# Performance work log

Measured on AMD Instinct MI355X. Metric: run time of the kernel, lower is better.

Reference implementation:

```python
import jax, jax.numpy as jnp
import numpy as np

D_MODEL = 4096
N_EXPERTS = 64
LN_EPS = 1e-5


def setup_inputs() -> dict:
    key = jax.random.key(0)
    k_x, k_w, k_b = jax.random.split(key, 3)
    x = jax.random.normal(k_x, (4, 4096, D_MODEL), dtype=jnp.float32)
    # LayerNorm affine params (torch defaults: ones / zeros)
    gamma = jnp.ones((D_MODEL,), dtype=jnp.float32)
    beta = jnp.zeros((D_MODEL,), dtype=jnp.float32)
    # Linear(d_model, n): weight (n, d), bias (n) — kaiming-uniform-ish init
    bound = 1.0 / np.sqrt(D_MODEL)
    W = jax.random.uniform(k_w, (N_EXPERTS, D_MODEL), dtype=jnp.float32, minval=-bound, maxval=bound)
    b = jax.random.uniform(k_b, (N_EXPERTS,), dtype=jnp.float32, minval=-bound, maxval=bound)
    return {"x": x, "gamma": gamma, "beta": beta, "W": W, "b": b, "top_k": 2}


def reference(x, gamma, beta, W, b, top_k):
    # LayerNorm over last dim
    mu = jnp.mean(x, axis=-1, keepdims=True)
    var = jnp.mean(jnp.square(x - mu), axis=-1, keepdims=True)
    xn = (x - mu) * jax.lax.rsqrt(var + LN_EPS) * gamma + beta
    # Gate projection: (B,T,d) @ (d,n) -> (B,T,n)
    logits = jnp.einsum('btd,nd->btn', xn, W) + b
    weights = jax.nn.softmax(logits, axis=-1)  # (B,T,n)
    k = min(int(top_k), weights.shape[-1])
    topk_vals, indices = jax.lax.top_k(weights, k)  # (B,T,k)
    # scatter top-k values back to dense (B,T,n), then renormalize
    onehot = jax.nn.one_hot(indices, weights.shape[-1], dtype=weights.dtype)  # (B,T,k,n)
    sparse_w = jnp.einsum('btkn,btk->btn', onehot, topk_vals)
    sparse_w = sparse_w / (jnp.sum(sparse_w, axis=-1, keepdims=True) + 1e-8)
    # load-balance (entropy) loss on dense weights
    mean_w = jnp.mean(weights, axis=(0, 1))  # (n,)
    lb_loss = -jnp.sum(mean_w * jnp.log(mean_w + 1e-8))
    return sparse_w, indices, lb_loss
```

## Files before the change

kernel.cpp:

```cpp
#include <hip/hip_runtime.h>
#include <math.h>

#define D_MODEL 4096
#define N_EXP   64
#define N_ROWS  16384
#define LN_EPS  1e-5f
#define TMB     64
#define NBLK    (N_ROWS / TMB)

typedef __attribute__((ext_vector_type(4))) float f32x4;
typedef __attribute__((ext_vector_type(8))) short s16x8;

struct U4 { unsigned v[4]; };

__device__ __forceinline__ unsigned pkt(float a, float b) {
  unsigned ua = __builtin_bit_cast(unsigned, a);
  unsigned ub = __builtin_bit_cast(unsigned, b);
  return (ua >> 16) | (ub & 0xffff0000u);
}
__device__ __forceinline__ float lo2f(unsigned p) { return __builtin_bit_cast(float, p << 16); }
__device__ __forceinline__ float hi2f(unsigned p) { return __builtin_bit_cast(float, p & 0xffff0000u); }

__device__ __forceinline__ void split8(const float* f, U4& u1, U4& u2, U4& u3) {
#pragma unroll
  for (int i = 0; i < 4; ++i) {
    const float a = f[2 * i], b = f[2 * i + 1];
    const unsigned p1 = pkt(a, b);
    const float ra = a - lo2f(p1), rb = b - hi2f(p1);
    const unsigned p2 = pkt(ra, rb);
    const float sa = ra - lo2f(p2), sb = rb - hi2f(p2);
    u1.v[i] = p1; u2.v[i] = p2; u3.v[i] = pkt(sa, sb);
  }
}


__global__ __launch_bounds__(64) void prep_bpre(
    const float* __restrict__ W, const float* __restrict__ gamma,
    float* __restrict__ Bpre)
{
  const int b = blockIdx.x;
  const int kb32 = b >> 2, j0 = b & 3;
  const int L = threadIdx.x, q = L >> 4, c = L & 15;
  const int n  = j0 * 16 + c;
  const int k0 = kb32 * 32 + q * 8;
  const float4 w0 = *(const float4*)(W + (size_t)n * D_MODEL + k0);
  const float4 w1 = *(const float4*)(W + (size_t)n * D_MODEL + k0 + 4);
  const float4 g0 = *(const float4*)(gamma + k0);
  const float4 g1 = *(const float4*)(gamma + k0 + 4);
  float f[8] = {w0.x * g0.x, w0.y * g0.y, w0.z * g0.z, w0.w * g0.w,
                w1.x * g1.x, w1.y * g1.y, w1.z * g1.z, w1.w * g1.w};
  U4 u1, u2, u3;
  split8(f, u1, u2, u3);
  const size_t base = ((size_t)kb32 * 12 + j0 * 3) * 64 + L;
  *(float4*)(Bpre + (base + 0 * 64) * 4) = __builtin_bit_cast(float4, u1);
  *(float4*)(Bpre + (base + 1 * 64) * 4) = __builtin_bit_cast(float4, u2);
  *(float4*)(Bpre + (base + 2 * 64) * 4) = __builtin_bit_cast(float4, u3);
}

__global__ __launch_bounds__(256) void prep_gc(
    const float* __restrict__ W, const float* __restrict__ gamma,
    const float* __restrict__ beta, const float* __restrict__ bias,
    float* __restrict__ G, float* __restrict__ C)
{
  const int e = blockIdx.x, t = threadIdx.x;
  float sg = 0.f, sb = 0.f;
#pragma unroll
  for (int i = 0; i < 4; ++i) {
    const int d = (i * 256 + t) * 4;
    const float4 wv = *(const float4*)(W + (size_t)e * D_MODEL + d);
    const float4 gv = *(const float4*)(gamma + d);
    const float4 bv = *(const float4*)(beta + d);
    sg += wv.x * gv.x + wv.y * gv.y + wv.z * gv.z + wv.w * gv.w;
    sb += wv.x * bv.x + wv.y * bv.y + wv.z * bv.z + wv.w * bv.w;
  }
#pragma unroll
  for (int o = 32; o > 0; o >>= 1) {
    sg += __shfl_xor(sg, o, 64);
    sb += __shfl_xor(sb, o, 64);
  }
  __shared__ float rg_[4], rb_[4];
  const int wid = t >> 6, ln = t & 63;
  if (ln == 0) { rg_[wid] = sg; rb_[wid] = sb; }
  __syncthreads();
  if (t == 0) {
    G[e] = rg_[0] + rg_[1] + rg_[2] + rg_[3];
    C[e] = rb_[0] + rb_[1] + rb_[2] + rb_[3] + bias[e];
  }
}

__device__ __forceinline__ void loadA(const float* aptr, int kb, float4 A[8]) {
  const float* ap = aptr + (size_t)kb * 128;
#pragma unroll
  for (int s = 0; s < 4; ++s) {
    A[2 * s]     = *(const float4*)(ap + s * 32);
    A[2 * s + 1] = *(const float4*)(ap + s * 32 + 4);
  }
}

__device__ __forceinline__ void loadB(const float* __restrict__ Bpre, int kb32, int L,
                                      s16x8 bf[4][3]) {
#pragma unroll
  for (int j0 = 0; j0 < 4; ++j0)
#pragma unroll
    for (int tt = 0; tt < 3; ++tt) {
      const float4 bv = *(const float4*)(Bpre + (((size_t)kb32 * 12 + j0 * 3 + tt) * 64 + L) * 4);
      bf[j0][tt] = __builtin_bit_cast(s16x8, bv);
    }
}

__device__ __forceinline__ void compute_chunk(
    const float* __restrict__ Bpre, const float* aptr, int kb, int next_kb, int L,
    const float4 Acur[8], float4 Anext[8], f32x4 acc[4], float& Sp, float& Qp)
{
  const int PA[6] = {0, 0, 1, 0, 1, 2};
  const int PB[6] = {0, 1, 0, 2, 1, 0};
  s16x8 bf[2][4][3];
  loadB(Bpre, kb * 4, L, bf[0]);
  loadA(aptr, next_kb, Anext);
#pragma unroll
  for (int s = 0; s < 4; ++s) {
    if (s < 3) loadB(Bpre, kb * 4 + s + 1, L, bf[(s + 1) & 1]);
    const float4 a0 = Acur[2 * s], a1 = Acur[2 * s + 1];
    const float f[8] = {a0.x, a0.y, a0.z, a0.w, a1.x, a1.y, a1.z, a1.w};
#pragma unroll
    for (int i = 0; i < 8; ++i) { Sp += f[i]; Qp = fmaf(f[i], f[i], Qp); }
    U4 u1, u2, u3;
    split8(f, u1, u2, u3);
    const s16x8 af[3] = {__builtin_bit_cast(s16x8, u1),
                         __builtin_bit_cast(s16x8, u2),
                         __builtin_bit_cast(s16x8, u3)};
#pragma unroll
    for (int p = 0; p < 6; ++p)
#pragma unroll
      for (int j0 = 0; j0 < 4; ++j0)
        acc[j0] = __builtin_amdgcn_mfma_f32_16x16x32_bf16(af[PA[p]], bf[s & 1][j0][PB[p]],
                                                          acc[j0], 0, 0, 0);
  }
}

__global__ __launch_bounds__(256, 1) void router_main(
    const float* __restrict__ x, const float* __restrict__ Bpre,
    const float* __restrict__ G, const float* __restrict__ C,
    float* __restrict__ out_sw, float* __restrict__ out_idx,
    float* __restrict__ out_partials, int k)
{
  const int t = threadIdx.x, w = t >> 6, L = t & 63;
  const int q = L >> 4, c = L & 15;
  const int blk = blockIdx.x;
  const int row0 = blk * TMB + w * 16;

  const float* aptr = x + (size_t)(row0 + c) * D_MODEL + q * 8;

  f32x4 acc[4];
#pragma unroll
  for (int j0 = 0; j0 < 4; ++j0) acc[j0] = (f32x4){0.f, 0.f, 0.f, 0.f};
  float Sp = 0.f, Qp = 0.f;

  float4 A0[8], A1[8];
  loadA(aptr, 0, A0);

  for (int kb = 0; kb < 32; kb += 2) {
    compute_chunk(Bpre, aptr, kb,     kb + 1,              L, A0, A1, acc, Sp, Qp);
    compute_chunk(Bpre, aptr, kb + 1, (kb + 2) & 31,       L, A1, A0, acc, Sp, Qp);
  }

#pragma unroll
  for (int o = 16; o <= 32; o <<= 1) {
    Sp += __shfl_xor(Sp, o, 64);
    Qp += __shfl_xor(Qp, o, 64);
  }
  const float mu = Sp * (1.f / D_MODEL);
  const float rs = rsqrtf(Qp * (1.f / D_MODEL) - mu * mu + LN_EPS);

  float Gv[4], Cv[4];
#pragma unroll
  for (int j0 = 0; j0 < 4; ++j0) { Gv[j0] = G[16 * j0 + c]; Cv[j0] = C[16 * j0 + c]; }

  float mw[4] = {0.f, 0.f, 0.f, 0.f};
#pragma unroll
  for (int i = 0; i < 4; ++i) {
    const int rloc = 4 * q + i;
    const int row  = row0 + rloc;
    const float mui = __shfl(mu, rloc, 64);
    const float rsi = __shfl(rs, rloc, 64);
    float l[4];
#pragma unroll
    for (int j0 = 0; j0 < 4; ++j0)
      l[j0] = rsi * (acc[j0][i] - mui * Gv[j0]) + Cv[j0];
    float mx = fmaxf(fmaxf(l[0], l[1]), fmaxf(l[2], l[3]));
#pragma unroll
    for (int o = 1; o < 16; o <<= 1) mx = fmaxf(mx, __shfl_xor(mx, o, 64));
    float p[4], ss = 0.f;
#pragma unroll
    for (int j0 = 0; j0 < 4; ++j0) { p[j0] = __expf(l[j0] - mx); ss += p[j0]; }
#pragma unroll
    for (int o = 1; o < 16; o <<= 1) ss += __shfl_xor(ss, o, 64);
    float wv[4];
#pragma unroll
    for (int j0 = 0; j0 < 4; ++j0) { wv[j0] = p[j0] / ss; mw[j0] += wv[j0]; }

    int ch[4];
    float denom = 0.f;
    for (int kk = 0; kk < k && kk < 4; ++kk) {
      float vb = -1.f; int eb = 1 << 30;
#pragma unroll
      for (int j0 = 0; j0 < 4; ++j0) {
        const int e = 16 * j0 + c;
        bool skip = false;
        for (int z = 0; z < kk; ++z) skip |= (ch[z] == e);
        const float cand = skip ? -1.f : wv[j0];
        if (cand > vb || (cand == vb && e < eb)) { vb = cand; eb = e; }
      }
#pragma unroll
      for (int o = 1; o < 16; o <<= 1) {
        const float ov = __shfl_xor(vb, o, 64);
        const int   oe = __shfl_xor(eb, o, 64);
        if (ov > vb || (ov == vb && oe < eb)) { vb = ov; eb = oe; }
      }
      ch[kk] = eb; denom += vb;
      if (c == 0) out_idx[(size_t)row * k + kk] = (float)eb;
    }
    denom += 1e-8f;
#pragma unroll
    for (int j0 = 0; j0 < 4; ++j0) {
      const int e = 16 * j0 + c;
      bool sel = false;
      for (int z = 0; z < k && z < 4; ++z) sel |= (ch[z] == e);
      out_sw[(size_t)row * N_EXP + e] = sel ? wv[j0] / denom : 0.f;
    }
  }

#pragma unroll
  for (int j0 = 0; j0 < 4; ++j0)
#pragma unroll
    for (int o = 16; o <= 32; o <<= 1) mw[j0] += __shfl_xor(mw[j0], o, 64);
  __shared__ float sm[4][64];
  if (q == 0) {
#pragma unroll
    for (int j0 = 0; j0 < 4; ++j0) sm[w][16 * j0 + c] = mw[j0];
  }
  __syncthreads();
  if (t < 64)
    out_partials[blk * 64 + t] = sm[0][t] + sm[1][t] + sm[2][t] + sm[3][t];
}

__global__ __launch_bounds__(256) void loss_kernel(
    const float* __restrict__ partials, float* __restrict__ out_loss)
{
  const int t = threadIdx.x, e = t & 63, qq = t >> 6;
  float s = 0.f;
#pragma unroll 8
  for (int b = 0; b < 64; ++b) s += partials[(qq * 64 + b) * 64 + e];
  __shared__ float sh[256];
  sh[t] = s;
  __syncthreads();
  if (t < 64) {
    const float m = (sh[t] + sh[64 + t] + sh[128 + t] + sh[192 + t]) * (1.f / N_ROWS);
    float v = -m * logf(m + 1e-8f);
#pragma unroll
    for (int o = 32; o > 0; o >>= 1) v += __shfl_xor(v, o, 64);
    if (t == 0) out_loss[0] = v;
  }
}

extern "C" void kernel_launch(void* const* d_in, const int* in_sizes, int n_in,
                              void* d_out, int out_size, void* d_ws, size_t ws_size,
                              hipStream_t stream)
{
  const float* x     = (const float*)d_in[0];
  const float* gamma = (const float*)d_in[1];
  const float* beta  = (const float*)d_in[2];
  const float* W     = (const float*)d_in[3];
  const float* bias  = (const float*)d_in[4];

  float* ws       = (float*)d_ws;
  float* Bpre     = ws;
  float* G        = ws + 393216;
  float* C        = ws + 393280;
  float* partials = ws + 393344;

  int k = (out_size - N_ROWS * N_EXP - 1) / N_ROWS;
  if (k < 1) k = 1;
  if (k > 4) k = 4;

  float* out      = (float*)d_out;
  float* out_sw   = out;
  float* out_idx  = out + (size_t)N_ROWS * N_EXP;
  float* out_loss = out + (size_t)N_ROWS * N_EXP + (size_t)N_ROWS * k;

  hipLaunchKernelGGL(prep_bpre, dim3(512), dim3(64), 0, stream, W, gamma, Bpre);
  hipLaunchKernelGGL(prep_gc, dim3(N_EXP), dim3(256), 0, stream, W, gamma, beta, bias, G, C);
  hipLaunchKernelGGL(router_main, dim3(NBLK), dim3(256), 0, stream,
                     x, Bpre, G, C, out_sw, out_idx, partials, k);
  hipLaunchKernelGGL(loss_kernel, dim3(1), dim3(256), 0, stream, partials, out_loss);
}
```

Measured before the change: 508.1 us.

## Split K across four waves per row group and reduce partials in LDS

Each 16-row group is now processed by four waves, each covering a quarter of the model dimension. The accumulators and LayerNorm sums are reduced through shared memory before the softmax/top-k epilogue. Block size doubles, blocks halve in row count, and the loss kernel reads twice as many partials. The aim is more waves in flight to hide global load latency on a memory-bound GEMV-like pass. The costs are an LDS reduction and barrier, and the tighter launch bounds risk register spills.

```diff
diff --git a/kernel.cpp b/kernel.cpp
--- a/kernel.cpp
+++ b/kernel.cpp
@@ -5,7 +5,7 @@
 #define N_EXP   64
 #define N_ROWS  16384
 #define LN_EPS  1e-5f
-#define TMB     64
+#define TMB     32
 #define NBLK    (N_ROWS / TMB)
 
 typedef __attribute__((ext_vector_type(4))) float f32x4;
@@ -138,7 +138,7 @@
   }
 }
 
-__global__ __launch_bounds__(256, 1) void router_main(
+__global__ __launch_bounds__(512, 4) void router_main(
     const float* __restrict__ x, const float* __restrict__ Bpre,
     const float* __restrict__ G, const float* __restrict__ C,
     float* __restrict__ out_sw, float* __restrict__ out_idx,
@@ -146,8 +146,10 @@
 {
   const int t = threadIdx.x, w = t >> 6, L = t & 63;
   const int q = L >> 4, c = L & 15;
+  const int g = w >> 2;
+  const int ks = w & 3;
   const int blk = blockIdx.x;
-  const int row0 = blk * TMB + w * 16;
+  const int row0 = blk * TMB + g * 16;
 
   const float* aptr = x + (size_t)(row0 + c) * D_MODEL + q * 8;
 
@@ -157,11 +159,13 @@
   float Sp = 0.f, Qp = 0.f;
 
   float4 A0[8], A1[8];
-  loadA(aptr, 0, A0);
-
-  for (int kb = 0; kb < 32; kb += 2) {
-    compute_chunk(Bpre, aptr, kb,     kb + 1,              L, A0, A1, acc, Sp, Qp);
-    compute_chunk(Bpre, aptr, kb + 1, (kb + 2) & 31,       L, A1, A0, acc, Sp, Qp);
+  const int kb0 = ks * 8;
+  loadA(aptr, kb0, A0);
+
+  for (int kb = kb0; kb < kb0 + 8; kb += 2) {
+    const int nxt = (kb + 2 < kb0 + 8) ? (kb + 2) : kb0;
+    compute_chunk(Bpre, aptr, kb,     kb + 1, L, A0, A1, acc, Sp, Qp);
+    compute_chunk(Bpre, aptr, kb + 1, nxt,    L, A1, A0, acc, Sp, Qp);
   }
 
 #pragma unroll
@@ -169,79 +173,103 @@
     Sp += __shfl_xor(Sp, o, 64);
     Qp += __shfl_xor(Qp, o, 64);
   }
-  const float mu = Sp * (1.f / D_MODEL);
-  const float rs = rsqrtf(Qp * (1.f / D_MODEL) - mu * mu + LN_EPS);
-
-  float Gv[4], Cv[4];
-#pragma unroll
-  for (int j0 = 0; j0 < 4; ++j0) { Gv[j0] = G[16 * j0 + c]; Cv[j0] = C[16 * j0 + c]; }
-
-  float mw[4] = {0.f, 0.f, 0.f, 0.f};
-#pragma unroll
-  for (int i = 0; i < 4; ++i) {
-    const int rloc = 4 * q + i;
-    const int row  = row0 + rloc;
-    const float mui = __shfl(mu, rloc, 64);
-    const float rsi = __shfl(rs, rloc, 64);
-    float l[4];
+
+  __shared__ float red[6][64][19];
+  __shared__ float sm[2][64];
+  if (ks != 0) {
+    float* dst = &red[g * 3 + (ks - 1)][L][0];
 #pragma unroll
     for (int j0 = 0; j0 < 4; ++j0)
-      l[j0] = rsi * (acc[j0][i] - mui * Gv[j0]) + Cv[j0];
-    float mx = fmaxf(fmaxf(l[0], l[1]), fmaxf(l[2], l[3]));
-#pragma unroll
-    for (int o = 1; o < 16; o <<= 1) mx = fmaxf(mx, __shfl_xor(mx, o, 64));
-    float p[4], ss = 0.f;
-#pragma unroll
-    for (int j0 = 0; j0 < 4; ++j0) { p[j0] = __expf(l[j0] - mx); ss += p[j0]; }
-#pragma unroll
-    for (int o = 1; o < 16; o <<= 1) ss += __shfl_xor(ss, o, 64);
-    float wv[4];
-#pragma unroll
-    for (int j0 = 0; j0 < 4; ++j0) { wv[j0] = p[j0] / ss; mw[j0] += wv[j0]; }
-
-    int ch[4];
-    float denom = 0.f;
-    for (int kk = 0; kk < k && kk < 4; ++kk) {
-      float vb = -1.f; int eb = 1 << 30;
+#pragma unroll
+      for (int i = 0; i < 4; ++i) dst[j0 * 4 + i] = acc[j0][i];
+    dst[16] = Sp; dst[17] = Qp;
+  }
+  __syncthreads();
+
+  if (ks == 0) {
+#pragma unroll
+    for (int src = 0; src < 3; ++src) {
+      const float* sp_ = &red[g * 3 + src][L][0];
+#pragma unroll
+      for (int j0 = 0; j0 < 4; ++j0)
+#pragma unroll
+        for (int i = 0; i < 4; ++i) acc[j0][i] += sp_[j0 * 4 + i];
+      Sp += sp_[16]; Qp += sp_[17];
+    }
+
+    const float mu = Sp * (1.f / D_MODEL);
+    const float rs = rsqrtf(Qp * (1.f / D_MODEL) - mu * mu + LN_EPS);
+
+    float Gv[4], Cv[4];
+#pragma unroll
+    for (int j0 = 0; j0 < 4; ++j0) { Gv[j0] = G[16 * j0 + c]; Cv[j0] = C[16 * j0 + c]; }
+
+    float mw[4] = {0.f, 0.f, 0.f, 0.f};
+#pragma unroll
+    for (int i = 0; i < 4; ++i) {
+      const int rloc = 4 * q + i;
+      const int row  = row0 + rloc;
+      const float mui = __shfl(mu, rloc, 64);
+      const float rsi = __shfl(rs, rloc, 64);
+      float l[4];
+#pragma unroll
+      for (int j0 = 0; j0 < 4; ++j0)
+        l[j0] = rsi * (acc[j0][i] - mui * Gv[j0]) + Cv[j0];
+      float mx = fmaxf(fmaxf(l[0], l[1]), fmaxf(l[2], l[3]));
+#pragma unroll
+      for (int o = 1; o < 16; o <<= 1) mx = fmaxf(mx, __shfl_xor(mx, o, 64));
+      float p[4], ss = 0.f;
+#pragma unroll
+      for (int j0 = 0; j0 < 4; ++j0) { p[j0] = __expf(l[j0] - mx); ss += p[j0]; }
+#pragma unroll
+      for (int o = 1; o < 16; o <<= 1) ss += __shfl_xor(ss, o, 64);
+      float wv[4];
+#pragma unroll
+      for (int j0 = 0; j0 < 4; ++j0) { wv[j0] = p[j0] / ss; mw[j0] += wv[j0]; }
+
+      int ch[4];
+      float denom = 0.f;
+      for (int kk = 0; kk < k && kk < 4; ++kk) {
+        float vb = -1.f; int eb = 1 << 30;
+#pragma unroll
+        for (int j0 = 0; j0 < 4; ++j0) {
+          const int e = 16 * j0 + c;
+          bool skip = false;
+          for (int z = 0; z < kk; ++z) skip |= (ch[z] == e);
+          const float cand = skip ? -1.f : wv[j0];
+          if (cand > vb || (cand == vb && e < eb)) { vb = cand; eb = e; }
+        }
+#pragma unroll
+        for (int o = 1; o < 16; o <<= 1) {
+          const float ov = __shfl_xor(vb, o, 64);
+          const int   oe = __shfl_xor(eb, o, 64);
+          if (ov > vb || (ov == vb && oe < eb)) { vb = ov; eb = oe; }
+        }
+        ch[kk] = eb; denom += vb;
+        if (c == 0) out_idx[(size_t)row * k + kk] = (float)eb;
+      }
+      denom += 1e-8f;
 #pragma unroll
       for (int j0 = 0; j0 < 4; ++j0) {
         const int e = 16 * j0 + c;
-        bool skip = false;
-        for (int z = 0; z < kk; ++z) skip |= (ch[z] == e);
-        const float cand = skip ? -1.f : wv[j0];
-        if (cand > vb || (cand == vb && e < eb)) { vb = cand; eb = e; }
+        bool sel = false;
+        for (int z = 0; z < k && z < 4; ++z) sel |= (ch[z] == e);
+        out_sw[(size_t)row * N_EXP + e] = sel ? wv[j0] / denom : 0.f;
       }
-#pragma unroll
-      for (int o = 1; o < 16; o <<= 1) {
-        const float ov = __shfl_xor(vb, o, 64);
-        const int   oe = __shfl_xor(eb, o, 64);
-        if (ov > vb || (ov == vb && oe < eb)) { vb = ov; eb = oe; }
-      }
-      ch[kk] = eb; denom += vb;
-      if (c == 0) out_idx[(size_t)row * k + kk] = (float)eb;
     }
-    denom += 1e-8f;
-#pragma unroll
-    for (int j0 = 0; j0 < 4; ++j0) {
-      const int e = 16 * j0 + c;
-      bool sel = false;
-      for (int z = 0; z < k && z < 4; ++z) sel |= (ch[z] == e);
-      out_sw[(size_t)row * N_EXP + e] = sel ? wv[j0] / denom : 0.f;
+
+#pragma unroll
+    for (int j0 = 0; j0 < 4; ++j0)
+#pragma unroll
+      for (int o = 16; o <= 32; o <<= 1) mw[j0] += __shfl_xor(mw[j0], o, 64);
+    if (q == 0) {
+#pragma unroll
+      for (int j0 = 0; j0 < 4; ++j0) sm[g][16 * j0 + c] = mw[j0];
     }
-  }
-
-#pragma unroll
-  for (int j0 = 0; j0 < 4; ++j0)
-#pragma unroll
-    for (int o = 16; o <= 32; o <<= 1) mw[j0] += __shfl_xor(mw[j0], o, 64);
-  __shared__ float sm[4][64];
-  if (q == 0) {
-#pragma unroll
-    for (int j0 = 0; j0 < 4; ++j0) sm[w][16 * j0 + c] = mw[j0];
   }
   __syncthreads();
   if (t < 64)
-    out_partials[blk * 64 + t] = sm[0][t] + sm[1][t] + sm[2][t] + sm[3][t];
+    out_partials[blk * 64 + t] = sm[0][t] + sm[1][t];
 }
 
 __global__ __launch_bounds__(256) void loss_kernel(
@@ -250,7 +278,7 @@
   const int t = threadIdx.x, e = t & 63, qq = t >> 6;
   float s = 0.f;
 #pragma unroll 8
-  for (int b = 0; b < 64; ++b) s += partials[(qq * 64 + b) * 64 + e];
+  for (int b = 0; b < 128; ++b) s += partials[(qq * 128 + b) * 64 + e];
   __shared__ float sh[256];
   sh[t] = s;
   __syncthreads();
@@ -290,7 +318,7 @@
 
   hipLaunchKernelGGL(prep_bpre, dim3(512), dim3(64), 0, stream, W, gamma, Bpre);
   hipLaunchKernelGGL(prep_gc, dim3(N_EXP), dim3(256), 0, stream, W, gamma, beta, bias, G, C);
-  hipLaunchKernelGGL(router_main, dim3(NBLK), dim3(256), 0, stream,
+  hipLaunchKernelGGL(router_main, dim3(NBLK), dim3(512), 0, stream,
                      x, Bpre, G, C, out_sw, out_idx, partials, k);
   hipLaunchKernelGGL(loss_kernel, dim3(1), dim3(256), 0, stream, partials, out_loss);
 }
```

New measurement: 501.3 us. Within noise of the previous version (-1.3%).

## Stage gate-weight tiles in LDS via global_load_lds with double buffering

Applied to the files above, without the earlier changes.

Before, each of the four waves in a block read the same pre-split bf16 weight fragments straight from global memory. Now each wave copies a quarter of each k-chunk into a double-buffered LDS array using direct global-to-LDS loads, and all waves read B from LDS. This cuts the repeated L2/global traffic for the weight operand by about four times per block. In exchange it adds workgroup barriers every chunk and about 96 KB of LDS per block, and it removes the register-level prefetch of B.

```diff
diff --git a/kernel.cpp b/kernel.cpp
--- a/kernel.cpp
+++ b/kernel.cpp
@@ -97,29 +97,37 @@
   }
 }
 
-__device__ __forceinline__ void loadB(const float* __restrict__ Bpre, int kb32, int L,
-                                      s16x8 bf[4][3]) {
-#pragma unroll
-  for (int j0 = 0; j0 < 4; ++j0)
-#pragma unroll
-    for (int tt = 0; tt < 3; ++tt) {
-      const float4 bv = *(const float4*)(Bpre + (((size_t)kb32 * 12 + j0 * 3 + tt) * 64 + L) * 4);
-      bf[j0][tt] = __builtin_bit_cast(s16x8, bv);
-    }
-}
-
-__device__ __forceinline__ void compute_chunk(
-    const float* __restrict__ Bpre, const float* aptr, int kb, int next_kb, int L,
-    const float4 Acur[8], float4 Anext[8], f32x4 acc[4], float& Sp, float& Qp)
+__device__ __forceinline__ void gload_lds16(const float* g, const float4* l) {
+  __builtin_amdgcn_global_load_lds(
+      (const __attribute__((address_space(1))) void*)(g),
+      (__attribute__((address_space(3))) void*)(l),
+      16, 0, 0);
+}
+
+__device__ __forceinline__ void stage_chunk(const float* __restrict__ Bpre,
+                                            float4* ldsbuf, int kb, int w, int L)
+{
+  const float* src = Bpre + (((size_t)(kb * 4 + w) * 12) * 64 + L) * 4;
+  float4* dst = ldsbuf + (size_t)(w * 12) * 64;
+#pragma unroll
+  for (int i = 0; i < 12; ++i)
+    gload_lds16(src + (size_t)i * 256, dst + (size_t)i * 64);
+}
+
+__device__ __forceinline__ void compute_chunk_lds(
+    const float4* __restrict__ buf, int L,
+    const float4 Acur[8], f32x4 acc[4], float& Sp, float& Qp)
 {
   const int PA[6] = {0, 0, 1, 0, 1, 2};
   const int PB[6] = {0, 1, 0, 2, 1, 0};
-  s16x8 bf[2][4][3];
-  loadB(Bpre, kb * 4, L, bf[0]);
-  loadA(aptr, next_kb, Anext);
 #pragma unroll
   for (int s = 0; s < 4; ++s) {
-    if (s < 3) loadB(Bpre, kb * 4 + s + 1, L, bf[(s + 1) & 1]);
+    s16x8 bf[4][3];
+#pragma unroll
+    for (int j0 = 0; j0 < 4; ++j0)
+#pragma unroll
+      for (int tt = 0; tt < 3; ++tt)
+        bf[j0][tt] = __builtin_bit_cast(s16x8, buf[(size_t)(s * 12 + j0 * 3 + tt) * 64 + L]);
     const float4 a0 = Acur[2 * s], a1 = Acur[2 * s + 1];
     const float f[8] = {a0.x, a0.y, a0.z, a0.w, a1.x, a1.y, a1.z, a1.w};
 #pragma unroll
@@ -133,7 +141,7 @@
     for (int p = 0; p < 6; ++p)
 #pragma unroll
       for (int j0 = 0; j0 < 4; ++j0)
-        acc[j0] = __builtin_amdgcn_mfma_f32_16x16x32_bf16(af[PA[p]], bf[s & 1][j0][PB[p]],
+        acc[j0] = __builtin_amdgcn_mfma_f32_16x16x32_bf16(af[PA[p]], bf[j0][PB[p]],
                                                           acc[j0], 0, 0, 0);
   }
 }
@@ -151,6 +159,8 @@
 
   const float* aptr = x + (size_t)(row0 + c) * D_MODEL + q * 8;
 
+  __shared__ float4 Bl[2][48 * 64];
+
   f32x4 acc[4];
 #pragma unroll
   for (int j0 = 0; j0 < 4; ++j0) acc[j0] = (f32x4){0.f, 0.f, 0.f, 0.f};
@@ -158,10 +168,19 @@
 
   float4 A0[8], A1[8];
   loadA(aptr, 0, A0);
+  stage_chunk(Bpre, Bl[0], 0, w, L);
+  __syncthreads();
 
   for (int kb = 0; kb < 32; kb += 2) {
-    compute_chunk(Bpre, aptr, kb,     kb + 1,              L, A0, A1, acc, Sp, Qp);
-    compute_chunk(Bpre, aptr, kb + 1, (kb + 2) & 31,       L, A1, A0, acc, Sp, Qp);
+    stage_chunk(Bpre, Bl[1], kb + 1, w, L);
+    loadA(aptr, kb + 1, A1);
+    compute_chunk_lds(Bl[0], L, A0, acc, Sp, Qp);
+    __syncthreads();
+
+    if (kb + 2 < 32) stage_chunk(Bpre, Bl[0], kb + 2, w, L);
+    loadA(aptr, (kb + 2) & 31, A0);
+    compute_chunk_lds(Bl[1], L, A1, acc, Sp, Qp);
+    __syncthreads();
   }
 
 #pragma unroll
```

Result: faster. 423.2 us (-16.7%).

## Stage gate weights into per-wave LDS ring via direct global-to-LDS loads

Applied to the files above, without the earlier changes.

Replaces register-held prefetch of the pre-split bf16 weight fragments with async global_load_lds transfers into a per-wave double-buffered LDS ring. The fragments are then read with explicit ds_read_b128, and manual waitcnt plus sched_barrier ordering sets the pipeline. Activation prefetch shrinks to one 8-float chunk per step instead of a 32-float block, which lowers register pressure and interleaves loads with MFMA work. The hand-coded vmcnt/lgkmcnt counts assume a specific instruction order, so a compiler reorder could race. Each wave now issues many small steps with a full LDS wait per step.

```diff
diff --git a/kernel.cpp b/kernel.cpp
--- a/kernel.cpp
+++ b/kernel.cpp
@@ -7,6 +7,7 @@
 #define LN_EPS  1e-5f
 #define TMB     64
 #define NBLK    (N_ROWS / TMB)
+#define NK32    128
 
 typedef __attribute__((ext_vector_type(4))) float f32x4;
 typedef __attribute__((ext_vector_type(8))) short s16x8;
@@ -88,54 +89,75 @@
   }
 }
 
-__device__ __forceinline__ void loadA(const float* aptr, int kb, float4 A[8]) {
-  const float* ap = aptr + (size_t)kb * 128;
-#pragma unroll
-  for (int s = 0; s < 4; ++s) {
-    A[2 * s]     = *(const float4*)(ap + s * 32);
-    A[2 * s + 1] = *(const float4*)(ap + s * 32 + 4);
-  }
-}
-
-__device__ __forceinline__ void loadB(const float* __restrict__ Bpre, int kb32, int L,
-                                      s16x8 bf[4][3]) {
-#pragma unroll
-  for (int j0 = 0; j0 < 4; ++j0)
-#pragma unroll
-    for (int tt = 0; tt < 3; ++tt) {
-      const float4 bv = *(const float4*)(Bpre + (((size_t)kb32 * 12 + j0 * 3 + tt) * 64 + L) * 4);
-      bf[j0][tt] = __builtin_bit_cast(s16x8, bv);
-    }
-}
-
-__device__ __forceinline__ void compute_chunk(
-    const float* __restrict__ Bpre, const float* aptr, int kb, int next_kb, int L,
-    const float4 Acur[8], float4 Anext[8], f32x4 acc[4], float& Sp, float& Qp)
-{
+__device__ __forceinline__ void gload_lds16(const float* g, float4* l) {
+  __builtin_amdgcn_global_load_lds(
+      (const __attribute__((address_space(1))) void*)(g),
+      (__attribute__((address_space(3))) void*)(l),
+      16, 0, 0);
+}
+
+__device__ __forceinline__ void stage12(const float* __restrict__ Bpre,
+                                        float4* st, int nk, int L)
+{
+  const float* src = Bpre + ((size_t)nk * 12 * 64 + L) * 4;
+#pragma unroll
+  for (int i = 0; i < 12; ++i)
+    gload_lds16(src + (size_t)i * 256, st + i * 64);
+}
+
+__device__ __forceinline__ void loadA(const float* aptr, int nk, float4 A[2]) {
+  A[0] = *(const float4*)(aptr + (size_t)nk * 32);
+  A[1] = *(const float4*)(aptr + (size_t)nk * 32 + 4);
+}
+
+#define DSR(d, b, OFF) \
+  asm volatile("ds_read_b128 %0, %1 offset:" #OFF : "=v"(d) : "v"(b))
+
+__device__ __forceinline__ void step_one(
+    const float* __restrict__ Bpre, const float* aptr,
+    float4* stOther, unsigned rbase, int jn1, int jn2, int L,
+    float4 AC[2], f32x4 acc[4], float& Sp, float& Qp)
+{
+  asm volatile("s_waitcnt vmcnt(2)");
+  __builtin_amdgcn_sched_barrier(0);
+  const float4 a0 = AC[0], a1 = AC[1];
+  const float fv[8] = {a0.x, a0.y, a0.z, a0.w, a1.x, a1.y, a1.z, a1.w};
+#pragma unroll
+  for (int i = 0; i < 8; ++i) { Sp += fv[i]; Qp = fmaf(fv[i], fv[i], Qp); }
+  U4 u1, u2, u3;
+  split8(fv, u1, u2, u3);
+  const s16x8 af[3] = {__builtin_bit_cast(s16x8, u1),
+                       __builtin_bit_cast(s16x8, u2),
+                       __builtin_bit_cast(s16x8, u3)};
+  __builtin_amdgcn_sched_barrier(0);
+  stage12(Bpre, stOther, jn1, L);
+  __builtin_amdgcn_sched_barrier(0);
+  loadA(aptr, jn2, AC);
+  __builtin_amdgcn_sched_barrier(0);
+  f32x4 bfr[12];
+  DSR(bfr[0],  rbase, 0);
+  DSR(bfr[1],  rbase, 1024);
+  DSR(bfr[2],  rbase, 2048);
+  DSR(bfr[3],  rbase, 3072);
+  DSR(bfr[4],  rbase, 4096);
+  DSR(bfr[5],  rbase, 5120);
+  DSR(bfr[6],  rbase, 6144);
+  DSR(bfr[7],  rbase, 7168);
+  DSR(bfr[8],  rbase, 8192);
+  DSR(bfr[9],  rbase, 9216);
+  DSR(bfr[10], rbase, 10240);
+  DSR(bfr[11], rbase, 11264);
+  asm volatile("s_waitcnt lgkmcnt(0)");
+  __builtin_amdgcn_sched_barrier(0);
   const int PA[6] = {0, 0, 1, 0, 1, 2};
   const int PB[6] = {0, 1, 0, 2, 1, 0};
-  s16x8 bf[2][4][3];
-  loadB(Bpre, kb * 4, L, bf[0]);
-  loadA(aptr, next_kb, Anext);
-#pragma unroll
-  for (int s = 0; s < 4; ++s) {
-    if (s < 3) loadB(Bpre, kb * 4 + s + 1, L, bf[(s + 1) & 1]);
-    const float4 a0 = Acur[2 * s], a1 = Acur[2 * s + 1];
-    const float f[8] = {a0.x, a0.y, a0.z, a0.w, a1.x, a1.y, a1.z, a1.w};
-#pragma unroll
-    for (int i = 0; i < 8; ++i) { Sp += f[i]; Qp = fmaf(f[i], f[i], Qp); }
-    U4 u1, u2, u3;
-    split8(f, u1, u2, u3);
-    const s16x8 af[3] = {__builtin_bit_cast(s16x8, u1),
-                         __builtin_bit_cast(s16x8, u2),
-                         __builtin_bit_cast(s16x8, u3)};
-#pragma unroll
-    for (int p = 0; p < 6; ++p)
-#pragma unroll
-      for (int j0 = 0; j0 < 4; ++j0)
-        acc[j0] = __builtin_amdgcn_mfma_f32_16x16x32_bf16(af[PA[p]], bf[s & 1][j0][PB[p]],
-                                                          acc[j0], 0, 0, 0);
-  }
+#pragma unroll
+  for (int p = 0; p < 6; ++p)
+#pragma unroll
+    for (int j0 = 0; j0 < 4; ++j0)
+      acc[j0] = __builtin_amdgcn_mfma_f32_16x16x32_bf16(
+          af[PA[p]], __builtin_bit_cast(s16x8, bfr[j0 * 3 + PB[p]]),
+          acc[j0], 0, 0, 0);
 }
 
 __global__ __launch_bounds__(256, 1) void router_main(
@@ -151,18 +173,38 @@
 
   const float* aptr = x + (size_t)(row0 + c) * D_MODEL + q * 8;
 
+  __shared__ float4 ring[4][2][768];
+  __shared__ float smf[4][64];
+
+  float4* st0 = &ring[w][0][0];
+  float4* st1 = &ring[w][1][0];
+  const unsigned rb0 = (unsigned)(unsigned long long)
+      (__attribute__((address_space(3))) void*)&ring[w][0][L];
+  const unsigned rb1 = (unsigned)(unsigned long long)
+      (__attribute__((address_space(3))) void*)&ring[w][1][L];
+
   f32x4 acc[4];
 #pragma unroll
   for (int j0 = 0; j0 < 4; ++j0) acc[j0] = (f32x4){0.f, 0.f, 0.f, 0.f};
   float Sp = 0.f, Qp = 0.f;
 
-  float4 A0[8], A1[8];
-  loadA(aptr, 0, A0);
-
-  for (int kb = 0; kb < 32; kb += 2) {
-    compute_chunk(Bpre, aptr, kb,     kb + 1,              L, A0, A1, acc, Sp, Qp);
-    compute_chunk(Bpre, aptr, kb + 1, (kb + 2) & 31,       L, A1, A0, acc, Sp, Qp);
-  }
+  float4 Ae[2], Ao[2];
+
+  loadA(aptr, 0, Ae);
+  __builtin_amdgcn_sched_barrier(0);
+  stage12(Bpre, st0, 0, L);
+  __builtin_amdgcn_sched_barrier(0);
+  loadA(aptr, 1, Ao);
+  __builtin_amdgcn_sched_barrier(0);
+
+  for (int j = 0; j < NK32; j += 2) {
+    step_one(Bpre, aptr, st1, rb0,
+             (j + 1) & (NK32 - 1), (j + 2) & (NK32 - 1), L, Ae, acc, Sp, Qp);
+    step_one(Bpre, aptr, st0, rb1,
+             (j + 2) & (NK32 - 1), (j + 3) & (NK32 - 1), L, Ao, acc, Sp, Qp);
+  }
+
+  __syncthreads();
 
 #pragma unroll
   for (int o = 16; o <= 32; o <<= 1) {
@@ -234,14 +276,13 @@
   for (int j0 = 0; j0 < 4; ++j0)
 #pragma unroll
     for (int o = 16; o <= 32; o <<= 1) mw[j0] += __shfl_xor(mw[j0], o, 64);
-  __shared__ float sm[4][64];
   if (q == 0) {
 #pragma unroll
-    for (int j0 = 0; j0 < 4; ++j0) sm[w][16 * j0 + c] = mw[j0];
+    for (int j0 = 0; j0 < 4; ++j0) smf[w][16 * j0 + c] = mw[j0];
   }
   __syncthreads();
   if (t < 64)
-    out_partials[blk * 64 + t] = sm[0][t] + sm[1][t] + sm[2][t] + sm[3][t];
+    out_partials[blk * 64 + t] = smf[0][t] + smf[1][t] + smf[2][t] + smf[3][t];
 }
 
 __global__ __launch_bounds__(256) void loss_kernel(
```

Result: faster. 445.8 us (-12.3%).
